# Optimization experiments

Measured on AMD Instinct MI355X. Metric: run time of the kernel, lower is better.

Reference implementation:

```python
import jax, jax.numpy as jnp
import numpy as np

B, G, K, H, NC = 128, 12000, 512, 64, 100
FP = 2048
ALPHA = 0.1
STEPS = 10

def setup_inputs() -> dict:
    key = jax.random.key(0)
    ks = jax.random.split(key, 10)
    ctl = jax.random.normal(ks[0], (B, G), jnp.float32)
    # drug targets: sparse binary indicator per gene
    drug_targets = (jax.random.uniform(ks[1], (B, G)) < 0.01).astype(jnp.float32)
    cell_idx = jax.random.randint(ks[2], (B,), 0, NC, dtype=jnp.int32)
    drug_fp = jax.random.normal(ks[3], (B, FP), jnp.float32)  # unused in forward
    # gene->module membership (sparse-ish binary), ensure each module non-empty via deg clamp in model
    M = (jax.random.uniform(ks[4], (G, K)) < 0.02).astype(jnp.float32)
    # row-stochastic module adjacency for stable diffusion
    Araw = jax.random.uniform(ks[5], (K, K), jnp.float32)
    A = Araw / jnp.sum(Araw, axis=1, keepdims=True)
    W_in = jax.random.normal(ks[6], (2, H), jnp.float32) * 0.5
    b_in = jnp.zeros((H,), jnp.float32)
    cell_emb = jax.random.normal(ks[7], (NC, H), jnp.float32) * 0.02
    W_out = jax.random.normal(ks[8], (H, 1), jnp.float32) * 0.1
    b_out = jnp.zeros((1,), jnp.float32)
    return {"ctl": ctl, "drug_targets": drug_targets, "cell_idx": cell_idx,
            "drug_fp": drug_fp, "M": M, "A": A, "W_in": W_in, "b_in": b_in,
            "cell_emb": cell_emb, "W_out": W_out, "b_out": b_out}

def reference(ctl, drug_targets, cell_idx, drug_fp, M, A, W_in, b_in, cell_emb, W_out, b_out):
    # module degree (clamped) as in __init__
    mod_deg = jnp.maximum(jnp.sum(M, axis=0), 1.0)            # [K]
    x_gene = jnp.stack([ctl, drug_targets], axis=-1)          # [B,G,2]
    x_mod = jnp.einsum('gk,bgh->bkh', M, x_gene) / mod_deg[None, :, None]  # [B,K,2]
    S = jax.nn.relu(x_mod @ W_in + b_in)                      # [B,K,H]
    # 10-step personalized-PageRank-style diffusion over modules
    def step(Z, _):
        Z = (1.0 - ALPHA) * jnp.einsum('bkh,kl->blh', Z, A) + ALPHA * S
        return Z, None
    Z, _ = jax.lax.scan(step, S, None, length=STEPS)          # [B,K,H]
    h_gene = jnp.einsum('gk,bkh->bgh', M, Z)                  # [B,G,H]
    h_gene = h_gene + cell_emb[cell_idx][:, None, :]          # add cell embedding
    y = (h_gene @ W_out + b_out)[..., 0]                      # [B,G]
    return y
```

## Files before the change

### kernel.cpp

```cpp
#include <hip/hip_runtime.h>

#define B_    128
#define G_    12000
#define GP    12288
#define K_    512
#define H_    64
#define NSEG  24
#define SEGG  512
#define BKT   64
#define NGT   192

typedef __attribute__((ext_vector_type(8))) short bf16x8;
typedef __attribute__((ext_vector_type(4))) float f32x4;

__device__ __forceinline__ unsigned short f2bf(float x) {
    union { float f; unsigned u; } v; v.f = x;
    unsigned r = (v.u + 0x7FFFu + ((v.u >> 16) & 1u)) >> 16;
    return (unsigned short)r;
}
__device__ __forceinline__ float bf2f(unsigned short b) {
    union { float f; unsigned u; } v; v.u = ((unsigned)b) << 16;
    return v.f;
}

__device__ __forceinline__ void mm_body(int k0, int l0, float* __restrict__ sm,
        const float* __restrict__ Aop, const float* __restrict__ Bop,
        const float* __restrict__ Cop, const float* __restrict__ Dop,
        float alpha, float beta, float* __restrict__ O, float* __restrict__ O2) {
    float (*Xa)[68] = (float(*)[68])sm;
    float (*Xb)[36] = (float(*)[36])(sm + 2176);
    int tid = threadIdx.x;
    int kg = tid & 15, lg = tid >> 4;
    float acc[2][2] = {};
    for (int jj = 0; jj < K_; jj += 64) {
#pragma unroll
        for (int i = 0; i < 2; ++i) {
            int lin = tid + i * 256;
            int r = lin >> 4, c4 = lin & 15;
            *(float4*)&Xa[r][c4 * 4] =
                *(const float4*)&Aop[(size_t)(l0 + r) * K_ + jj + c4 * 4];
        }
#pragma unroll
        for (int i = 0; i < 2; ++i) {
            int lin = tid + i * 256;
            int r = lin >> 3, c4 = lin & 7;
            *(float4*)&Xb[r][c4 * 4] =
                *(const float4*)&Bop[(size_t)(jj + r) * K_ + k0 + c4 * 4];
        }
        __syncthreads();
#pragma unroll 8
        for (int j = 0; j < 64; ++j) {
            float xa0 = Xa[lg * 2][j], xa1 = Xa[lg * 2 + 1][j];
            float xb0 = Xb[j][kg * 2], xb1 = Xb[j][kg * 2 + 1];
            acc[0][0] = fmaf(xa0, xb0, acc[0][0]);
            acc[0][1] = fmaf(xa0, xb1, acc[0][1]);
            acc[1][0] = fmaf(xa1, xb0, acc[1][0]);
            acc[1][1] = fmaf(xa1, xb1, acc[1][1]);
        }
        __syncthreads();
    }
#pragma unroll
    for (int i = 0; i < 2; ++i) {
        size_t idx = (size_t)(l0 + lg * 2 + i) * K_ + k0 + kg * 2;
        float2 v;
        v.x = alpha * acc[i][0];
        v.y = alpha * acc[i][1];
        if (beta != 0.0f) {
            float2 cc = *(const float2*)&Cop[idx];
            v.x = fmaf(beta, cc.x, v.x);
            v.y = fmaf(beta, cc.y, v.y);
        }
        *(float2*)&O[idx] = v;
        if (O2) {
            float2 dd = *(const float2*)&Dop[idx];
            float2 w2; w2.x = v.x + dd.x; w2.y = v.y + dd.y;
            *(float2*)&O2[idx] = w2;
        }
    }
}

__device__ __forceinline__ void panel_body(int l, float* __restrict__ sm,
        const float* __restrict__ W, const float* __restrict__ src,
        float* __restrict__ out) {
    float* Wr  = sm;
    float* red = sm + 512;
    int tid = threadIdx.x;
    if (tid < 128)
        ((float4*)Wr)[tid] = ((const float4*)&W[(size_t)l * K_])[tid];
    __syncthreads();
    int b = tid & 127, seg = tid >> 7;
    int kb = seg * 256;
    float a0 = 0.f, a1 = 0.f, a2 = 0.f, a3 = 0.f;
#pragma unroll 4
    for (int kk = 0; kk < 256; kk += 4) {
        int k = kb + kk;
        a0 = fmaf(Wr[k + 0], src[(k + 0) * B_ + b], a0);
        a1 = fmaf(Wr[k + 1], src[(k + 1) * B_ + b], a1);
        a2 = fmaf(Wr[k + 2], src[(k + 2) * B_ + b], a2);
        a3 = fmaf(Wr[k + 3], src[(k + 3) * B_ + b], a3);
    }
    red[seg * 128 + b] = (a0 + a1) + (a2 + a3);
    __syncthreads();
    if (tid < 128)
        out[l * B_ + b] = red[b] + red[128 + b];
}

__global__ __launch_bounds__(256) void k_pre(
        const float* __restrict__ ctl, const float* __restrict__ dt,
        const float* __restrict__ M, const float* __restrict__ A,
        const int* __restrict__ cidx, const float* __restrict__ cemb,
        const float* __restrict__ W_out, const float* __restrict__ b_out,
        unsigned short* __restrict__ XpT, unsigned short* __restrict__ MTb,
        unsigned short* __restrict__ Mb, int* __restrict__ pdeg,
        float* __restrict__ AT, float* __restrict__ U2,
        float* __restrict__ cvec) {
    int bid = blockIdx.x, tid = threadIdx.x;
    if (bid < 3072) {
        int p = bid / 12, chunk = bid % 12;
        int ch = p >> 7, b = p & 127;
        const float* src = (ch ? dt : ctl) + (size_t)b * G_;
        int g = chunk * 1024 + tid * 4;
        float x0 = 0.f, x1 = 0.f, x2 = 0.f, x3 = 0.f;
        if (g + 3 < G_) {
            float4 v = *(const float4*)&src[g];
            x0 = v.x; x1 = v.y; x2 = v.z; x3 = v.w;
        } else {
            if (g + 0 < G_) x0 = src[g + 0];
            if (g + 1 < G_) x1 = src[g + 1];
            if (g + 2 < G_) x2 = src[g + 2];
            if (g + 3 < G_) x3 = src[g + 3];
        }
        ushort4 hv;
        hv.x = f2bf(x0); hv.y = f2bf(x1); hv.z = f2bf(x2); hv.w = f2bf(x3);
        *(ushort4*)&XpT[(size_t)p * GP + g] = hv;
    } else if (bid < 4608) {
        __shared__ float t[64][65];
        __shared__ int csum[4][64];
        int id = bid - 3072;
        int gt = id % NGT, kt = id / NGT;
        int g0 = gt * 64, k0 = kt * 64;
        int tx = tid & 63, ty = tid >> 6;
        int cnt = 0;
#pragma unroll
        for (int j = 0; j < 16; ++j) {
            int g = g0 + ty + 4 * j;
            float v = (g < G_) ? M[(size_t)g * K_ + k0 + tx] : 0.0f;
            t[ty + 4 * j][tx] = v;
            Mb[(size_t)g * K_ + k0 + tx] = f2bf(v);
            cnt += (v != 0.0f);
        }
        csum[ty][tx] = cnt;
        __syncthreads();
        if (ty == 0)
            pdeg[(size_t)(k0 + tx) * NGT + gt] =
                csum[0][tx] + csum[1][tx] + csum[2][tx] + csum[3][tx];
#pragma unroll
        for (int j = 0; j < 16; ++j)
            MTb[(size_t)(k0 + ty + 4 * j) * GP + g0 + tx] =
                f2bf(t[tx][ty + 4 * j]);
    } else if (bid < 4864) {
        __shared__ float t[32][33];
        int id = bid - 4608;
        int x0 = (id & 15) * 32, y0 = (id >> 4) * 32;
        int tx = tid & 31, ty = tid >> 5;
#pragma unroll
        for (int j = 0; j < 4; ++j)
            t[ty + 8 * j][tx] = A[(size_t)(y0 + ty + 8 * j) * K_ + x0 + tx];
        __syncthreads();
#pragma unroll
        for (int j = 0; j < 4; ++j) {
            int row = x0 + ty + 8 * j, col = y0 + tx;
            float v = t[tx][ty + 8 * j];
            AT[(size_t)row * K_ + col] = v;
            U2[(size_t)row * K_ + col] = 0.09f * v + (row == col ? 0.1f : 0.0f);
        }
    } else {
        if (tid < B_) {
            int ci = cidx[tid];
            float acc = b_out[0];
#pragma unroll 8
            for (int h = 0; h < H_; ++h)
                acc = fmaf(cemb[ci * H_ + h], W_out[h], acc);
            cvec[tid] = acc;
        }
    }
}

__global__ __launch_bounds__(256) void k_gemm(
        const unsigned short* __restrict__ MTb, const unsigned short* __restrict__ XpT,
        float* __restrict__ Cp,
        const float* __restrict__ AT, const float* __restrict__ U2,
        float* __restrict__ M2, float* __restrict__ Yop) {
    __shared__ __align__(16) char smraw[36864];
    int bid = blockIdx.x, tid = threadIdx.x;
    if (bid < 192) {
        unsigned short (*Al)[72] = (unsigned short(*)[72])smraw;
        unsigned short (*Bl)[72] = (unsigned short(*)[72])(smraw + 18432);
        int tile = bid & 7, seg = bid >> 3;
        int m0 = (tile & 3) * 128, n0 = (tile >> 2) * 128;
        size_t gbase = (size_t)seg * SEGG;
        int wid = tid >> 6, lane = tid & 63;
        int wm = (wid >> 1) * 64, wn = (wid & 1) * 64;
        int r16 = lane & 15, kg8 = (lane >> 4) * 8;
        int ld_row = tid >> 3, ld_c8 = (tid & 7) * 8;
        f32x4 acc[4][4] = {};
        for (int kk = 0; kk < SEGG; kk += BKT) {
#pragma unroll
            for (int i = 0; i < 4; ++i) {
                int r = ld_row + 32 * i;
                *(uint4*)&Al[r][ld_c8] =
                    *(const uint4*)&MTb[(size_t)(m0 + r) * GP + gbase + kk + ld_c8];
                *(uint4*)&Bl[r][ld_c8] =
                    *(const uint4*)&XpT[(size_t)(n0 + r) * GP + gbase + kk + ld_c8];
            }
            __syncthreads();
#pragma unroll
            for (int ks = 0; ks < 2; ++ks) {
                bf16x8 af[4], bf[4];
#pragma unroll
                for (int mi = 0; mi < 4; ++mi)
                    af[mi] = *(const bf16x8*)&Al[wm + mi * 16 + r16][ks * 32 + kg8];
#pragma unroll
                for (int ni = 0; ni < 4; ++ni)
                    bf[ni] = *(const bf16x8*)&Bl[wn + ni * 16 + r16][ks * 32 + kg8];
#pragma unroll
                for (int mi = 0; mi < 4; ++mi)
#pragma unroll
                    for (int ni = 0; ni < 4; ++ni)
                        acc[mi][ni] = __builtin_amdgcn_mfma_f32_16x16x32_bf16(
                            af[mi], bf[ni], acc[mi][ni], 0, 0, 0);
            }
            __syncthreads();
        }
        float* C = Cp + (size_t)seg * (K_ * 256);
        int cr = (lane >> 4) * 4, cc = lane & 15;
#pragma unroll
        for (int mi = 0; mi < 4; ++mi)
#pragma unroll
            for (int ni = 0; ni < 4; ++ni) {
                size_t rb = (size_t)(m0 + wm + mi * 16 + cr) * 256
                          + (n0 + wn + ni * 16 + cc);
#pragma unroll
                for (int r = 0; r < 4; ++r)
                    C[rb + (size_t)r * 256] = acc[mi][ni][r];
            }
    } else {
        int id = bid - 192;
        mm_body((id & 15) * 32, (id >> 4) * 32, (float*)smraw,
                AT, AT, nullptr, U2, 0.81f, 0.0f, M2, Yop);
    }
}

__global__ __launch_bounds__(256) void k_red(
        const float* __restrict__ Cp, const int* __restrict__ pdeg,
        const float* __restrict__ W_in, const float* __restrict__ b_in,
        const float* __restrict__ W_out, float* __restrict__ sout,
        const float* __restrict__ M2, const float* __restrict__ U2,
        float* __restrict__ M4, float* __restrict__ U4) {
    __shared__ __align__(16) float sm[4480];
    int bid = blockIdx.x, tid = threadIdx.x;
    if (bid < 256) {
        int kloc = tid >> 7, b = tid & 127;
        int k = bid * 2 + kloc;
        int v = 0;
        if (b < 96)
            v = pdeg[(size_t)k * NGT + b] + pdeg[(size_t)k * NGT + 96 + b];
#pragma unroll
        for (int off = 32; off; off >>= 1) v += __shfl_down(v, off, 64);
        __shared__ int dsum[4];
        __shared__ float degs[2];
        if ((tid & 63) == 0) dsum[tid >> 6] = v;
        __syncthreads();
        if (tid < 2) degs[tid] = (float)(dsum[tid * 2] + dsum[tid * 2 + 1]);
        __syncthreads();
        float x0 = 0.f, x1 = 0.f;
#pragma unroll 4
        for (int s = 0; s < NSEG; ++s) {
            const float* Cb = Cp + (size_t)s * (K_ * 256) + (size_t)k * 256;
            x0 += Cb[b];
            x1 += Cb[128 + b];
        }
        float inv = 1.0f / fmaxf(degs[kloc], 1.0f);
        x0 *= inv; x1 *= inv;
        float s = 0.f;
#pragma unroll 8
        for (int h = 0; h < H_; ++h) {
            float vv = fmaf(x0, W_in[h], fmaf(x1, W_in[H_ + h], b_in[h]));
            vv = fmaxf(vv, 0.f);
            s = fmaf(vv, W_out[h], s);
        }
        sout[k * B_ + b] = s;
    } else {
        int id = bid - 256;
        int t = id & 255;
        if (id < 256)
            mm_body((t & 15) * 32, (t >> 4) * 32, sm, M2, M2, nullptr, nullptr,
                    1.0f, 0.0f, M4, nullptr);
        else
            mm_body((t & 15) * 32, (t >> 4) * 32, sm, M2, U2, U2, nullptr,
                    1.0f, 1.0f, U4, nullptr);
    }
}

__global__ __launch_bounds__(256) void k_p3(
        const float* __restrict__ M4, const float* __restrict__ U4,
        float* __restrict__ M8,
        const float* __restrict__ Yop, const float* __restrict__ sout,
        float* __restrict__ q, float* __restrict__ bb) {
    __shared__ __align__(16) float sm[4480];
    int bid = blockIdx.x;
    if (bid < 256) {
        mm_body((bid & 15) * 32, (bid >> 4) * 32, sm, M4, M4, nullptr, nullptr,
                1.0f, 0.0f, M8, nullptr);
    } else if (bid < 768) {
        panel_body(bid - 256, sm, Yop, sout, q);
    } else {
        panel_body(bid - 768, sm, U4, sout, bb);
    }
}

__global__ __launch_bounds__(1024) void k_zfin(
        const float* __restrict__ M8, const float* __restrict__ M4,
        const float* __restrict__ q, const float* __restrict__ bb,
        unsigned short* __restrict__ zbT) {
    __shared__ __align__(16) float Wr[4 * K_];
    __shared__ float red[8][2][128];
    int tid = threadIdx.x;
    int l0 = blockIdx.x * 2;
    if (tid < 256)
        ((float4*)Wr)[tid] = ((const float4*)&M8[(size_t)l0 * K_])[tid];
    else if (tid < 512)
        ((float4*)&Wr[2 * K_])[tid - 256] =
            ((const float4*)&M4[(size_t)l0 * K_])[tid - 256];
    __syncthreads();
    int b = tid & 127, seg = tid >> 7;
    int kb = seg * 64;
    float a0m = 0.f, a0u = 0.f, a1m = 0.f, a1u = 0.f;
#pragma unroll 8
    for (int kk = 0; kk < 64; ++kk) {
        int k = kb + kk;
        float qv = q[k * B_ + b];
        float bv = bb[k * B_ + b];
        a0m = fmaf(Wr[k], qv, a0m);
        a0u = fmaf(Wr[2 * K_ + k], bv, a0u);
        a1m = fmaf(Wr[K_ + k], qv, a1m);
        a1u = fmaf(Wr[3 * K_ + k], bv, a1u);
    }
    red[seg][0][b] = a0m + a0u;
    red[seg][1][b] = a1m + a1u;
    __syncthreads();
    if (tid < 256) {
        int row = tid >> 7, bi = tid & 127;
        float t = bb[(l0 + row) * B_ + bi];
#pragma unroll
        for (int u = 0; u < 8; ++u) t += red[u][row][bi];
        unsigned short hi = f2bf(t);
        unsigned short lo = f2bf(t - bf2f(hi));
        zbT[(size_t)bi * (2 * K_) + (l0 + row)]      = hi;
        zbT[(size_t)bi * (2 * K_) + K_ + (l0 + row)] = lo;
    }
}

__global__ __launch_bounds__(256) void k_yg(
        const unsigned short* __restrict__ Mb, const unsigned short* __restrict__ zbT,
        const float* __restrict__ cvec, float* __restrict__ y) {
    __shared__ __align__(16) unsigned short Al[64][72];
    __shared__ __align__(16) unsigned short Bh[128][72];
    __shared__ __align__(16) unsigned short Bl2[128][72];
    int tid = threadIdx.x;
    int g0 = blockIdx.x * 64;
    int wid = tid >> 6, lane = tid & 63;
    int wm = (wid >> 1) * 32, wn = (wid & 1) * 64;
    int r16 = lane & 15, kg8 = (lane >> 4) * 8;
    int ld_row = tid >> 3, ld_c8 = (tid & 7) * 8;
    f32x4 acc[2][4] = {};
    for (int kk = 0; kk < K_; kk += BKT) {
#pragma unroll
        for (int i = 0; i < 2; ++i) {
            int r = ld_row + 32 * i;
            *(uint4*)&Al[r][ld_c8] =
                *(const uint4*)&Mb[(size_t)(g0 + r) * K_ + kk + ld_c8];
        }
#pragma unroll
        for (int i = 0; i < 4; ++i) {
            int r = ld_row + 32 * i;
            *(uint4*)&Bh[r][ld_c8] =
                *(const uint4*)&zbT[(size_t)r * (2 * K_) + kk + ld_c8];
            *(uint4*)&Bl2[r][ld_c8] =
                *(const uint4*)&zbT[(size_t)r * (2 * K_) + K_ + kk + ld_c8];
        }
        __syncthreads();
#pragma unroll
        for (int ks = 0; ks < 2; ++ks) {
            bf16x8 af[2], bh[4], bl[4];
#pragma unroll
            for (int mi = 0; mi < 2; ++mi)
                af[mi] = *(const bf16x8*)&Al[wm + mi * 16 + r16][ks * 32 + kg8];
#pragma unroll
            for (int ni = 0; ni < 4; ++ni) {
                bh[ni] = *(const bf16x8*)&Bh[wn + ni * 16 + r16][ks * 32 + kg8];
                bl[ni] = *(const bf16x8*)&Bl2[wn + ni * 16 + r16][ks * 32 + kg8];
            }
#pragma unroll
            for (int mi = 0; mi < 2; ++mi)
#pragma unroll
                for (int ni = 0; ni < 4; ++ni) {
                    acc[mi][ni] = __builtin_amdgcn_mfma_f32_16x16x32_bf16(
                        af[mi], bh[ni], acc[mi][ni], 0, 0, 0);
                    acc[mi][ni] = __builtin_amdgcn_mfma_f32_16x16x32_bf16(
                        af[mi], bl[ni], acc[mi][ni], 0, 0, 0);
                }
        }
        __syncthreads();
    }
    int cr = (lane >> 4) * 4, cc = lane & 15;
#pragma unroll
    for (int ni = 0; ni < 4; ++ni) {
        int b = wn + ni * 16 + cc;
        float cv = cvec[b];
#pragma unroll
        for (int mi = 0; mi < 2; ++mi) {
            int g = g0 + wm + mi * 16 + cr;
            if (g < G_) {
                float4 o;
                o.x = acc[mi][ni][0] + cv;
                o.y = acc[mi][ni][1] + cv;
                o.z = acc[mi][ni][2] + cv;
                o.w = acc[mi][ni][3] + cv;
                *(float4*)&y[(size_t)b * G_ + g] = o;
            }
        }
    }
}

extern "C" void kernel_launch(void* const* d_in, const int* in_sizes, int n_in,
                              void* d_out, int out_size, void* d_ws, size_t ws_size,
                              hipStream_t stream) {
    const float* ctl   = (const float*)d_in[0];
    const float* dt    = (const float*)d_in[1];
    const int*   cidx  = (const int*)d_in[2];
    const float* M     = (const float*)d_in[4];
    const float* A     = (const float*)d_in[5];
    const float* W_in  = (const float*)d_in[6];
    const float* b_in  = (const float*)d_in[7];
    const float* cemb  = (const float*)d_in[8];
    const float* W_out = (const float*)d_in[9];
    const float* b_out = (const float*)d_in[10];
    float* y = (float*)d_out;

    char* ws = (char*)d_ws;
    size_t o = 0;
    auto take = [&](size_t bytes) { char* p = ws + o; o = (o + bytes + 255) & ~(size_t)255; return p; };
    unsigned short* XpT = (unsigned short*)take((size_t)256 * GP * 2);
    unsigned short* MTb = (unsigned short*)take((size_t)K_ * GP * 2);
    unsigned short* Mb  = (unsigned short*)take((size_t)GP * K_ * 2);
    unsigned short* zbT = (unsigned short*)take((size_t)B_ * 2 * K_ * 2);
    float* Cp   = (float*)take((size_t)NSEG * K_ * 256 * 4);
    int*   pdeg = (int*)  take((size_t)K_ * NGT * 4);
    float* cvec = (float*)take(B_ * 4);
    float* AT   = (float*)take((size_t)K_ * K_ * 4);
    float* U2   = (float*)take((size_t)K_ * K_ * 4);
    float* M2   = (float*)take((size_t)K_ * K_ * 4);
    float* Yop  = (float*)take((size_t)K_ * K_ * 4);
    float* M4   = (float*)take((size_t)K_ * K_ * 4);
    float* U4   = (float*)take((size_t)K_ * K_ * 4);
    float* M8   = (float*)take((size_t)K_ * K_ * 4);
    float* sout = (float*)take((size_t)K_ * B_ * 4);
    float* q    = (float*)take((size_t)K_ * B_ * 4);
    float* bb   = (float*)take((size_t)K_ * B_ * 4);
    (void)ws_size; (void)in_sizes; (void)n_in; (void)out_size;

    k_pre<<<4865, 256, 0, stream>>>(ctl, dt, M, A, cidx, cemb, W_out, b_out,
                                    XpT, MTb, Mb, pdeg, AT, U2, cvec);
    k_gemm<<<448, 256, 0, stream>>>(MTb, XpT, Cp, AT, U2, M2, Yop);
    k_red<<<768, 256, 0, stream>>>(Cp, pdeg, W_in, b_in, W_out, sout,
                                   M2, U2, M4, U4);
    k_p3<<<1280, 256, 0, stream>>>(M4, U4, M8, Yop, sout, q, bb);
    k_zfin<<<K_ / 2, 1024, 0, stream>>>(M8, M4, q, bb, zbT);
    k_yg<<<(G_ + 63) / 64, 256, 0, stream>>>(Mb, zbT, cvec, y);
}
```

Baseline: 98.73 us.

## Fuse six stage kernels into one cooperative persistent kernel with grid syncs

Replaces the six separate kernel launches with a single cooperative persistent kernel of 256 blocks that loops over each stage's jobs and separates stages with grid-wide syncs, keeping the old multi-launch path as a fallback. The aim is to remove per-launch overhead and the drain/fill gaps between kernels. The zfin stage is also reworked from 1024-thread blocks handling two rows to 256-thread blocks handling one row. The risk is that 256 persistent blocks underuse the GPU on the large stages such as the 4865-job preprocessing, and grid syncs carry their own cost.

```diff
diff --git a/kernel.cpp b/kernel.cpp
--- a/kernel.cpp
+++ b/kernel.cpp
@@ -1,4 +1,7 @@
 #include <hip/hip_runtime.h>
+#include <hip/hip_cooperative_groups.h>
+
+namespace cg = cooperative_groups;
 
 #define B_    128
 #define G_    12000
@@ -9,6 +12,7 @@
 #define SEGG  512
 #define BKT   64
 #define NGT   192
+#define NB    256
 
 typedef __attribute__((ext_vector_type(8))) short bf16x8;
 typedef __attribute__((ext_vector_type(4))) float f32x4;
@@ -22,6 +26,17 @@
     union { float f; unsigned u; } v; v.u = ((unsigned)b) << 16;
     return v.f;
 }
+
+struct Params {
+    const float *ctl, *dt, *M, *A;
+    const int* cidx;
+    const float *cemb, *W_out, *b_out, *W_in, *b_in;
+    unsigned short *XpT, *MTb, *Mb, *zbT;
+    float* Cp;
+    int* pdeg;
+    float *cvec, *AT, *U2, *M2, *Yop, *M4, *U4, *M8, *sout, *q, *bb;
+    float* y;
+};
 
 __device__ __forceinline__ void mm_body(int k0, int l0, float* __restrict__ sm,
         const float* __restrict__ Aop, const float* __restrict__ Bop,
@@ -105,20 +120,12 @@
         out[l * B_ + b] = red[b] + red[128 + b];
 }
 
-__global__ __launch_bounds__(256) void k_pre(
-        const float* __restrict__ ctl, const float* __restrict__ dt,
-        const float* __restrict__ M, const float* __restrict__ A,
-        const int* __restrict__ cidx, const float* __restrict__ cemb,
-        const float* __restrict__ W_out, const float* __restrict__ b_out,
-        unsigned short* __restrict__ XpT, unsigned short* __restrict__ MTb,
-        unsigned short* __restrict__ Mb, int* __restrict__ pdeg,
-        float* __restrict__ AT, float* __restrict__ U2,
-        float* __restrict__ cvec) {
-    int bid = blockIdx.x, tid = threadIdx.x;
-    if (bid < 3072) {
-        int p = bid / 12, chunk = bid % 12;
-        int ch = p >> 7, b = p & 127;
-        const float* src = (ch ? dt : ctl) + (size_t)b * G_;
+__device__ __forceinline__ void pre_job(int j, char* smraw, const Params& p) {
+    int tid = threadIdx.x;
+    if (j < 3072) {
+        int pp = j / 12, chunk = j % 12;
+        int ch = pp >> 7, b = pp & 127;
+        const float* src = (ch ? p.dt : p.ctl) + (size_t)b * G_;
         int g = chunk * 1024 + tid * 4;
         float x0 = 0.f, x1 = 0.f, x2 = 0.f, x3 = 0.f;
         if (g + 3 < G_) {
@@ -132,243 +139,187 @@
         }
         ushort4 hv;
         hv.x = f2bf(x0); hv.y = f2bf(x1); hv.z = f2bf(x2); hv.w = f2bf(x3);
-        *(ushort4*)&XpT[(size_t)p * GP + g] = hv;
-    } else if (bid < 4608) {
-        __shared__ float t[64][65];
-        __shared__ int csum[4][64];
-        int id = bid - 3072;
+        *(ushort4*)&p.XpT[(size_t)pp * GP + g] = hv;
+    } else if (j < 4608) {
+        float (*t)[65] = (float(*)[65])smraw;
+        int (*csum)[64] = (int(*)[64])(smraw + 16640);
+        int id = j - 3072;
         int gt = id % NGT, kt = id / NGT;
         int g0 = gt * 64, k0 = kt * 64;
         int tx = tid & 63, ty = tid >> 6;
         int cnt = 0;
 #pragma unroll
-        for (int j = 0; j < 16; ++j) {
-            int g = g0 + ty + 4 * j;
-            float v = (g < G_) ? M[(size_t)g * K_ + k0 + tx] : 0.0f;
-            t[ty + 4 * j][tx] = v;
-            Mb[(size_t)g * K_ + k0 + tx] = f2bf(v);
+        for (int jj = 0; jj < 16; ++jj) {
+            int g = g0 + ty + 4 * jj;
+            float v = (g < G_) ? p.M[(size_t)g * K_ + k0 + tx] : 0.0f;
+            t[ty + 4 * jj][tx] = v;
+            p.Mb[(size_t)g * K_ + k0 + tx] = f2bf(v);
             cnt += (v != 0.0f);
         }
         csum[ty][tx] = cnt;
         __syncthreads();
         if (ty == 0)
-            pdeg[(size_t)(k0 + tx) * NGT + gt] =
+            p.pdeg[(size_t)(k0 + tx) * NGT + gt] =
                 csum[0][tx] + csum[1][tx] + csum[2][tx] + csum[3][tx];
 #pragma unroll
-        for (int j = 0; j < 16; ++j)
-            MTb[(size_t)(k0 + ty + 4 * j) * GP + g0 + tx] =
-                f2bf(t[tx][ty + 4 * j]);
-    } else if (bid < 4864) {
-        __shared__ float t[32][33];
-        int id = bid - 4608;
+        for (int jj = 0; jj < 16; ++jj)
+            p.MTb[(size_t)(k0 + ty + 4 * jj) * GP + g0 + tx] =
+                f2bf(t[tx][ty + 4 * jj]);
+    } else if (j < 4864) {
+        float (*t)[33] = (float(*)[33])smraw;
+        int id = j - 4608;
         int x0 = (id & 15) * 32, y0 = (id >> 4) * 32;
         int tx = tid & 31, ty = tid >> 5;
 #pragma unroll
-        for (int j = 0; j < 4; ++j)
-            t[ty + 8 * j][tx] = A[(size_t)(y0 + ty + 8 * j) * K_ + x0 + tx];
-        __syncthreads();
-#pragma unroll
-        for (int j = 0; j < 4; ++j) {
-            int row = x0 + ty + 8 * j, col = y0 + tx;
-            float v = t[tx][ty + 8 * j];
-            AT[(size_t)row * K_ + col] = v;
-            U2[(size_t)row * K_ + col] = 0.09f * v + (row == col ? 0.1f : 0.0f);
+        for (int jj = 0; jj < 4; ++jj)
+            t[ty + 8 * jj][tx] = p.A[(size_t)(y0 + ty + 8 * jj) * K_ + x0 + tx];
+        __syncthreads();
+#pragma unroll
+        for (int jj = 0; jj < 4; ++jj) {
+            int row = x0 + ty + 8 * jj, col = y0 + tx;
+            float v = t[tx][ty + 8 * jj];
+            p.AT[(size_t)row * K_ + col] = v;
+            p.U2[(size_t)row * K_ + col] = 0.09f * v + (row == col ? 0.1f : 0.0f);
         }
     } else {
         if (tid < B_) {
-            int ci = cidx[tid];
-            float acc = b_out[0];
+            int ci = p.cidx[tid];
+            float acc = p.b_out[0];
 #pragma unroll 8
             for (int h = 0; h < H_; ++h)
-                acc = fmaf(cemb[ci * H_ + h], W_out[h], acc);
-            cvec[tid] = acc;
-        }
-    }
-}
-
-__global__ __launch_bounds__(256) void k_gemm(
-        const unsigned short* __restrict__ MTb, const unsigned short* __restrict__ XpT,
-        float* __restrict__ Cp,
-        const float* __restrict__ AT, const float* __restrict__ U2,
-        float* __restrict__ M2, float* __restrict__ Yop) {
-    __shared__ __align__(16) char smraw[36864];
-    int bid = blockIdx.x, tid = threadIdx.x;
-    if (bid < 192) {
-        unsigned short (*Al)[72] = (unsigned short(*)[72])smraw;
-        unsigned short (*Bl)[72] = (unsigned short(*)[72])(smraw + 18432);
-        int tile = bid & 7, seg = bid >> 3;
-        int m0 = (tile & 3) * 128, n0 = (tile >> 2) * 128;
-        size_t gbase = (size_t)seg * SEGG;
-        int wid = tid >> 6, lane = tid & 63;
-        int wm = (wid >> 1) * 64, wn = (wid & 1) * 64;
-        int r16 = lane & 15, kg8 = (lane >> 4) * 8;
-        int ld_row = tid >> 3, ld_c8 = (tid & 7) * 8;
-        f32x4 acc[4][4] = {};
-        for (int kk = 0; kk < SEGG; kk += BKT) {
-#pragma unroll
-            for (int i = 0; i < 4; ++i) {
-                int r = ld_row + 32 * i;
-                *(uint4*)&Al[r][ld_c8] =
-                    *(const uint4*)&MTb[(size_t)(m0 + r) * GP + gbase + kk + ld_c8];
-                *(uint4*)&Bl[r][ld_c8] =
-                    *(const uint4*)&XpT[(size_t)(n0 + r) * GP + gbase + kk + ld_c8];
-            }
-            __syncthreads();
-#pragma unroll
-            for (int ks = 0; ks < 2; ++ks) {
-                bf16x8 af[4], bf[4];
-#pragma unroll
-                for (int mi = 0; mi < 4; ++mi)
-                    af[mi] = *(const bf16x8*)&Al[wm + mi * 16 + r16][ks * 32 + kg8];
+                acc = fmaf(p.cemb[ci * H_ + h], p.W_out[h], acc);
+            p.cvec[tid] = acc;
+        }
+    }
+}
+
+__device__ __forceinline__ void gemm_job(int j, char* smraw, const Params& p) {
+    unsigned short (*Al)[72] = (unsigned short(*)[72])smraw;
+    unsigned short (*Bl)[72] = (unsigned short(*)[72])(smraw + 18432);
+    int tid = threadIdx.x;
+    int tile = j & 7, seg = j >> 3;
+    int m0 = (tile & 3) * 128, n0 = (tile >> 2) * 128;
+    size_t gbase = (size_t)seg * SEGG;
+    int wid = tid >> 6, lane = tid & 63;
+    int wm = (wid >> 1) * 64, wn = (wid & 1) * 64;
+    int r16 = lane & 15, kg8 = (lane >> 4) * 8;
+    int ld_row = tid >> 3, ld_c8 = (tid & 7) * 8;
+    f32x4 acc[4][4] = {};
+    for (int kk = 0; kk < SEGG; kk += BKT) {
+#pragma unroll
+        for (int i = 0; i < 4; ++i) {
+            int r = ld_row + 32 * i;
+            *(uint4*)&Al[r][ld_c8] =
+                *(const uint4*)&p.MTb[(size_t)(m0 + r) * GP + gbase + kk + ld_c8];
+            *(uint4*)&Bl[r][ld_c8] =
+                *(const uint4*)&p.XpT[(size_t)(n0 + r) * GP + gbase + kk + ld_c8];
+        }
+        __syncthreads();
+#pragma unroll
+        for (int ks = 0; ks < 2; ++ks) {
+            bf16x8 af[4], bf[4];
+#pragma unroll
+            for (int mi = 0; mi < 4; ++mi)
+                af[mi] = *(const bf16x8*)&Al[wm + mi * 16 + r16][ks * 32 + kg8];
+#pragma unroll
+            for (int ni = 0; ni < 4; ++ni)
+                bf[ni] = *(const bf16x8*)&Bl[wn + ni * 16 + r16][ks * 32 + kg8];
+#pragma unroll
+            for (int mi = 0; mi < 4; ++mi)
 #pragma unroll
                 for (int ni = 0; ni < 4; ++ni)
-                    bf[ni] = *(const bf16x8*)&Bl[wn + ni * 16 + r16][ks * 32 + kg8];
-#pragma unroll
-                for (int mi = 0; mi < 4; ++mi)
-#pragma unroll
-                    for (int ni = 0; ni < 4; ++ni)
-                        acc[mi][ni] = __builtin_amdgcn_mfma_f32_16x16x32_bf16(
-                            af[mi], bf[ni], acc[mi][ni], 0, 0, 0);
-            }
-            __syncthreads();
-        }
-        float* C = Cp + (size_t)seg * (K_ * 256);
-        int cr = (lane >> 4) * 4, cc = lane & 15;
-#pragma unroll
-        for (int mi = 0; mi < 4; ++mi)
-#pragma unroll
-            for (int ni = 0; ni < 4; ++ni) {
-                size_t rb = (size_t)(m0 + wm + mi * 16 + cr) * 256
-                          + (n0 + wn + ni * 16 + cc);
-#pragma unroll
-                for (int r = 0; r < 4; ++r)
-                    C[rb + (size_t)r * 256] = acc[mi][ni][r];
-            }
-    } else {
-        int id = bid - 192;
-        mm_body((id & 15) * 32, (id >> 4) * 32, (float*)smraw,
-                AT, AT, nullptr, U2, 0.81f, 0.0f, M2, Yop);
-    }
-}
-
-__global__ __launch_bounds__(256) void k_red(
-        const float* __restrict__ Cp, const int* __restrict__ pdeg,
-        const float* __restrict__ W_in, const float* __restrict__ b_in,
-        const float* __restrict__ W_out, float* __restrict__ sout,
-        const float* __restrict__ M2, const float* __restrict__ U2,
-        float* __restrict__ M4, float* __restrict__ U4) {
-    __shared__ __align__(16) float sm[4480];
-    int bid = blockIdx.x, tid = threadIdx.x;
-    if (bid < 256) {
-        int kloc = tid >> 7, b = tid & 127;
-        int k = bid * 2 + kloc;
-        int v = 0;
-        if (b < 96)
-            v = pdeg[(size_t)k * NGT + b] + pdeg[(size_t)k * NGT + 96 + b];
-#pragma unroll
-        for (int off = 32; off; off >>= 1) v += __shfl_down(v, off, 64);
-        __shared__ int dsum[4];
-        __shared__ float degs[2];
-        if ((tid & 63) == 0) dsum[tid >> 6] = v;
-        __syncthreads();
-        if (tid < 2) degs[tid] = (float)(dsum[tid * 2] + dsum[tid * 2 + 1]);
-        __syncthreads();
-        float x0 = 0.f, x1 = 0.f;
+                    acc[mi][ni] = __builtin_amdgcn_mfma_f32_16x16x32_bf16(
+                        af[mi], bf[ni], acc[mi][ni], 0, 0, 0);
+        }
+        __syncthreads();
+    }
+    float* C = p.Cp + (size_t)seg * (K_ * 256);
+    int cr = (lane >> 4) * 4, cc = lane & 15;
+#pragma unroll
+    for (int mi = 0; mi < 4; ++mi)
+#pragma unroll
+        for (int ni = 0; ni < 4; ++ni) {
+            size_t rb = (size_t)(m0 + wm + mi * 16 + cr) * 256
+                      + (n0 + wn + ni * 16 + cc);
+#pragma unroll
+            for (int r = 0; r < 4; ++r)
+                C[rb + (size_t)r * 256] = acc[mi][ni][r];
+        }
+}
+
+__device__ __forceinline__ void red_job(int j, const Params& p) {
+    __shared__ int dsum[4];
+    __shared__ float degs[2];
+    int tid = threadIdx.x;
+    int kloc = tid >> 7, b = tid & 127;
+    int k = j * 2 + kloc;
+    int v = 0;
+    if (b < 96)
+        v = p.pdeg[(size_t)k * NGT + b] + p.pdeg[(size_t)k * NGT + 96 + b];
+#pragma unroll
+    for (int off = 32; off; off >>= 1) v += __shfl_down(v, off, 64);
+    if ((tid & 63) == 0) dsum[tid >> 6] = v;
+    __syncthreads();
+    if (tid < 2) degs[tid] = (float)(dsum[tid * 2] + dsum[tid * 2 + 1]);
+    __syncthreads();
+    float x0 = 0.f, x1 = 0.f;
 #pragma unroll 4
-        for (int s = 0; s < NSEG; ++s) {
-            const float* Cb = Cp + (size_t)s * (K_ * 256) + (size_t)k * 256;
-            x0 += Cb[b];
-            x1 += Cb[128 + b];
-        }
-        float inv = 1.0f / fmaxf(degs[kloc], 1.0f);
-        x0 *= inv; x1 *= inv;
-        float s = 0.f;
+    for (int s = 0; s < NSEG; ++s) {
+        const float* Cb = p.Cp + (size_t)s * (K_ * 256) + (size_t)k * 256;
+        x0 += Cb[b];
+        x1 += Cb[128 + b];
+    }
+    float inv = 1.0f / fmaxf(degs[kloc], 1.0f);
+    x0 *= inv; x1 *= inv;
+    float s = 0.f;
 #pragma unroll 8
-        for (int h = 0; h < H_; ++h) {
-            float vv = fmaf(x0, W_in[h], fmaf(x1, W_in[H_ + h], b_in[h]));
-            vv = fmaxf(vv, 0.f);
-            s = fmaf(vv, W_out[h], s);
-        }
-        sout[k * B_ + b] = s;
-    } else {
-        int id = bid - 256;
-        int t = id & 255;
-        if (id < 256)
-            mm_body((t & 15) * 32, (t >> 4) * 32, sm, M2, M2, nullptr, nullptr,
-                    1.0f, 0.0f, M4, nullptr);
-        else
-            mm_body((t & 15) * 32, (t >> 4) * 32, sm, M2, U2, U2, nullptr,
-                    1.0f, 1.0f, U4, nullptr);
-    }
-}
-
-__global__ __launch_bounds__(256) void k_p3(
-        const float* __restrict__ M4, const float* __restrict__ U4,
-        float* __restrict__ M8,
-        const float* __restrict__ Yop, const float* __restrict__ sout,
-        float* __restrict__ q, float* __restrict__ bb) {
-    __shared__ __align__(16) float sm[4480];
-    int bid = blockIdx.x;
-    if (bid < 256) {
-        mm_body((bid & 15) * 32, (bid >> 4) * 32, sm, M4, M4, nullptr, nullptr,
-                1.0f, 0.0f, M8, nullptr);
-    } else if (bid < 768) {
-        panel_body(bid - 256, sm, Yop, sout, q);
-    } else {
-        panel_body(bid - 768, sm, U4, sout, bb);
-    }
-}
-
-__global__ __launch_bounds__(1024) void k_zfin(
-        const float* __restrict__ M8, const float* __restrict__ M4,
-        const float* __restrict__ q, const float* __restrict__ bb,
-        unsigned short* __restrict__ zbT) {
-    __shared__ __align__(16) float Wr[4 * K_];
-    __shared__ float red[8][2][128];
-    int tid = threadIdx.x;
-    int l0 = blockIdx.x * 2;
-    if (tid < 256)
-        ((float4*)Wr)[tid] = ((const float4*)&M8[(size_t)l0 * K_])[tid];
-    else if (tid < 512)
-        ((float4*)&Wr[2 * K_])[tid - 256] =
-            ((const float4*)&M4[(size_t)l0 * K_])[tid - 256];
+    for (int h = 0; h < H_; ++h) {
+        float vv = fmaf(x0, p.W_in[h], fmaf(x1, p.W_in[H_ + h], p.b_in[h]));
+        vv = fmaxf(vv, 0.f);
+        s = fmaf(vv, p.W_out[h], s);
+    }
+    p.sout[k * B_ + b] = s;
+    __syncthreads();
+}
+
+__device__ __forceinline__ void zfin_job(int l, char* smraw, const Params& p) {
+    float* Wr  = (float*)smraw;
+    float* red = (float*)smraw + 1024;
+    int tid = threadIdx.x;
+    if (tid < 128)
+        ((float4*)Wr)[tid] = ((const float4*)&p.M8[(size_t)l * K_])[tid];
+    else
+        ((float4*)Wr)[tid] = ((const float4*)&p.M4[(size_t)l * K_])[tid - 128];
     __syncthreads();
     int b = tid & 127, seg = tid >> 7;
-    int kb = seg * 64;
-    float a0m = 0.f, a0u = 0.f, a1m = 0.f, a1u = 0.f;
-#pragma unroll 8
-    for (int kk = 0; kk < 64; ++kk) {
+    int kb = seg * 256;
+    float a0 = 0.f, a1 = 0.f, a2 = 0.f, a3 = 0.f;
+#pragma unroll 4
+    for (int kk = 0; kk < 256; kk += 2) {
         int k = kb + kk;
-        float qv = q[k * B_ + b];
-        float bv = bb[k * B_ + b];
-        a0m = fmaf(Wr[k], qv, a0m);
-        a0u = fmaf(Wr[2 * K_ + k], bv, a0u);
-        a1m = fmaf(Wr[K_ + k], qv, a1m);
-        a1u = fmaf(Wr[3 * K_ + k], bv, a1u);
-    }
-    red[seg][0][b] = a0m + a0u;
-    red[seg][1][b] = a1m + a1u;
-    __syncthreads();
-    if (tid < 256) {
-        int row = tid >> 7, bi = tid & 127;
-        float t = bb[(l0 + row) * B_ + bi];
-#pragma unroll
-        for (int u = 0; u < 8; ++u) t += red[u][row][bi];
+        a0 = fmaf(Wr[k],           p.q [(size_t)k * B_ + b], a0);
+        a1 = fmaf(Wr[512 + k],     p.bb[(size_t)k * B_ + b], a1);
+        a2 = fmaf(Wr[k + 1],       p.q [(size_t)(k + 1) * B_ + b], a2);
+        a3 = fmaf(Wr[512 + k + 1], p.bb[(size_t)(k + 1) * B_ + b], a3);
+    }
+    red[seg * 128 + b] = (a0 + a1) + (a2 + a3);
+    __syncthreads();
+    if (tid < 128) {
+        float t = red[tid] + red[128 + tid] + p.bb[(size_t)l * B_ + tid];
         unsigned short hi = f2bf(t);
         unsigned short lo = f2bf(t - bf2f(hi));
-        zbT[(size_t)bi * (2 * K_) + (l0 + row)]      = hi;
-        zbT[(size_t)bi * (2 * K_) + K_ + (l0 + row)] = lo;
-    }
-}
-
-__global__ __launch_bounds__(256) void k_yg(
-        const unsigned short* __restrict__ Mb, const unsigned short* __restrict__ zbT,
-        const float* __restrict__ cvec, float* __restrict__ y) {
-    __shared__ __align__(16) unsigned short Al[64][72];
-    __shared__ __align__(16) unsigned short Bh[128][72];
-    __shared__ __align__(16) unsigned short Bl2[128][72];
-    int tid = threadIdx.x;
-    int g0 = blockIdx.x * 64;
+        p.zbT[(size_t)tid * (2 * K_) + l]      = hi;
+        p.zbT[(size_t)tid * (2 * K_) + K_ + l] = lo;
+    }
+    __syncthreads();
+}
+
+__device__ __forceinline__ void yg_job(int j, char* smraw, const Params& p) {
+    unsigned short (*Al)[72]  = (unsigned short(*)[72])smraw;
+    unsigned short (*Bh)[72]  = (unsigned short(*)[72])(smraw + 9216);
+    unsigned short (*Bl2)[72] = (unsigned short(*)[72])(smraw + 27648);
+    int tid = threadIdx.x;
+    int g0 = j * 64;
     int wid = tid >> 6, lane = tid & 63;
     int wm = (wid >> 1) * 32, wn = (wid & 1) * 64;
     int r16 = lane & 15, kg8 = (lane >> 4) * 8;
@@ -379,15 +330,15 @@
         for (int i = 0; i < 2; ++i) {
             int r = ld_row + 32 * i;
             *(uint4*)&Al[r][ld_c8] =
-                *(const uint4*)&Mb[(size_t)(g0 + r) * K_ + kk + ld_c8];
+                *(const uint4*)&p.Mb[(size_t)(g0 + r) * K_ + kk + ld_c8];
         }
 #pragma unroll
         for (int i = 0; i < 4; ++i) {
             int r = ld_row + 32 * i;
             *(uint4*)&Bh[r][ld_c8] =
-                *(const uint4*)&zbT[(size_t)r * (2 * K_) + kk + ld_c8];
+                *(const uint4*)&p.zbT[(size_t)r * (2 * K_) + kk + ld_c8];
             *(uint4*)&Bl2[r][ld_c8] =
-                *(const uint4*)&zbT[(size_t)r * (2 * K_) + K_ + kk + ld_c8];
+                *(const uint4*)&p.zbT[(size_t)r * (2 * K_) + K_ + kk + ld_c8];
         }
         __syncthreads();
 #pragma unroll
@@ -417,7 +368,7 @@
 #pragma unroll
     for (int ni = 0; ni < 4; ++ni) {
         int b = wn + ni * 16 + cc;
-        float cv = cvec[b];
+        float cv = p.cvec[b];
 #pragma unroll
         for (int mi = 0; mi < 2; ++mi) {
             int g = g0 + wm + mi * 16 + cr;
@@ -427,55 +378,160 @@
                 o.y = acc[mi][ni][1] + cv;
                 o.z = acc[mi][ni][2] + cv;
                 o.w = acc[mi][ni][3] + cv;
-                *(float4*)&y[(size_t)b * G_ + g] = o;
+                *(float4*)&p.y[(size_t)b * G_ + g] = o;
             }
         }
     }
+}
+
+__global__ __launch_bounds__(256, 2) void k_mega(Params p) {
+    static __shared__ __align__(16) char smem[46080];
+    cg::grid_group grid = cg::this_grid();
+    float* smf = (float*)smem;
+
+    for (int j = blockIdx.x; j < 4865; j += NB) {
+        __syncthreads();
+        pre_job(j, smem, p);
+    }
+    grid.sync();
+    for (int j = blockIdx.x; j < 448; j += NB) {
+        __syncthreads();
+        if (j < 192) gemm_job(j, smem, p);
+        else {
+            int id = j - 192;
+            mm_body((id & 15) * 32, (id >> 4) * 32, smf,
+                    p.AT, p.AT, nullptr, p.U2, 0.81f, 0.0f, p.M2, p.Yop);
+        }
+    }
+    grid.sync();
+    for (int j = blockIdx.x; j < 768; j += NB) {
+        __syncthreads();
+        if (j < 256) red_job(j, p);
+        else if (j < 512) {
+            int t = j - 256;
+            mm_body((t & 15) * 32, (t >> 4) * 32, smf, p.M2, p.M2,
+                    nullptr, nullptr, 1.0f, 0.0f, p.M4, nullptr);
+        } else {
+            int t = j - 512;
+            mm_body((t & 15) * 32, (t >> 4) * 32, smf, p.M2, p.U2,
+                    p.U2, nullptr, 1.0f, 1.0f, p.U4, nullptr);
+        }
+    }
+    grid.sync();
+    for (int j = blockIdx.x; j < 1280; j += NB) {
+        __syncthreads();
+        if (j < 256)
+            mm_body((j & 15) * 32, (j >> 4) * 32, smf, p.M4, p.M4,
+                    nullptr, nullptr, 1.0f, 0.0f, p.M8, nullptr);
+        else if (j < 768) panel_body(j - 256, smf, p.Yop, p.sout, p.q);
+        else              panel_body(j - 768, smf, p.U4, p.sout, p.bb);
+    }
+    grid.sync();
+    for (int j = blockIdx.x; j < 512; j += NB) {
+        __syncthreads();
+        zfin_job(j, smem, p);
+    }
+    grid.sync();
+    for (int j = blockIdx.x; j < (G_ + 63) / 64; j += NB) {
+        __syncthreads();
+        yg_job(j, smem, p);
+    }
+}
+
+__global__ __launch_bounds__(256) void kf_pre(Params p) {
+    static __shared__ __align__(16) char smem[17664];
+    pre_job(blockIdx.x, smem, p);
+}
+__global__ __launch_bounds__(256) void kf_gemm(Params p) {
+    static __shared__ __align__(16) char smem[36864];
+    int j = blockIdx.x;
+    if (j < 192) gemm_job(j, smem, p);
+    else {
+        int id = j - 192;
+        mm_body((id & 15) * 32, (id >> 4) * 32, (float*)smem,
+                p.AT, p.AT, nullptr, p.U2, 0.81f, 0.0f, p.M2, p.Yop);
+    }
+}
+__global__ __launch_bounds__(256) void kf_red(Params p) {
+    static __shared__ __align__(16) char smem[17920];
+    int j = blockIdx.x;
+    if (j < 256) red_job(j, p);
+    else if (j < 512) {
+        int t = j - 256;
+        mm_body((t & 15) * 32, (t >> 4) * 32, (float*)smem, p.M2, p.M2,
+                nullptr, nullptr, 1.0f, 0.0f, p.M4, nullptr);
+    } else {
+        int t = j - 512;
+        mm_body((t & 15) * 32, (t >> 4) * 32, (float*)smem, p.M2, p.U2,
+                p.U2, nullptr, 1.0f, 1.0f, p.U4, nullptr);
+    }
+}
+__global__ __launch_bounds__(256) void kf_p3(Params p) {
+    static __shared__ __align__(16) char smem[17920];
+    int j = blockIdx.x;
+    if (j < 256)
+        mm_body((j & 15) * 32, (j >> 4) * 32, (float*)smem, p.M4, p.M4,
+                nullptr, nullptr, 1.0f, 0.0f, p.M8, nullptr);
+    else if (j < 768) panel_body(j - 256, (float*)smem, p.Yop, p.sout, p.q);
+    else              panel_body(j - 768, (float*)smem, p.U4, p.sout, p.bb);
+}
+__global__ __launch_bounds__(256) void kf_zfin(Params p) {
+    static __shared__ __align__(16) char smem[5120];
+    zfin_job(blockIdx.x, smem, p);
+}
+__global__ __launch_bounds__(256) void kf_yg(Params p) {
+    static __shared__ __align__(16) char smem[46080];
+    yg_job(blockIdx.x, smem, p);
 }
 
 extern "C" void kernel_launch(void* const* d_in, const int* in_sizes, int n_in,
                               void* d_out, int out_size, void* d_ws, size_t ws_size,
                               hipStream_t stream) {
-    const float* ctl   = (const float*)d_in[0];
-    const float* dt    = (const float*)d_in[1];
-    const int*   cidx  = (const int*)d_in[2];
-    const float* M     = (const float*)d_in[4];
-    const float* A     = (const float*)d_in[5];
-    const float* W_in  = (const float*)d_in[6];
-    const float* b_in  = (const float*)d_in[7];
-    const float* cemb  = (const float*)d_in[8];
-    const float* W_out = (const float*)d_in[9];
-    const float* b_out = (const float*)d_in[10];
-    float* y = (float*)d_out;
+    Params p;
+    p.ctl   = (const float*)d_in[0];
+    p.dt    = (const float*)d_in[1];
+    p.cidx  = (const int*)d_in[2];
+    p.M     = (const float*)d_in[4];
+    p.A     = (const float*)d_in[5];
+    p.W_in  = (const float*)d_in[6];
+    p.b_in  = (const float*)d_in[7];
+    p.cemb  = (const float*)d_in[8];
+    p.W_out = (const float*)d_in[9];
+    p.b_out = (const float*)d_in[10];
+    p.y     = (float*)d_out;
 
     char* ws = (char*)d_ws;
     size_t o = 0;
-    auto take = [&](size_t bytes) { char* p = ws + o; o = (o + bytes + 255) & ~(size_t)255; return p; };
-    unsigned short* XpT = (unsigned short*)take((size_t)256 * GP * 2);
-    unsigned short* MTb = (unsigned short*)take((size_t)K_ * GP * 2);
-    unsigned short* Mb  = (unsigned short*)take((size_t)GP * K_ * 2);
-    unsigned short* zbT = (unsigned short*)take((size_t)B_ * 2 * K_ * 2);
-    float* Cp   = (float*)take((size_t)NSEG * K_ * 256 * 4);
-    int*   pdeg = (int*)  take((size_t)K_ * NGT * 4);
-    float* cvec = (float*)take(B_ * 4);
-    float* AT   = (float*)take((size_t)K_ * K_ * 4);
-    float* U2   = (float*)take((size_t)K_ * K_ * 4);
-    float* M2   = (float*)take((size_t)K_ * K_ * 4);
-    float* Yop  = (float*)take((size_t)K_ * K_ * 4);
-    float* M4   = (float*)take((size_t)K_ * K_ * 4);
-    float* U4   = (float*)take((size_t)K_ * K_ * 4);
-    float* M8   = (float*)take((size_t)K_ * K_ * 4);
-    float* sout = (float*)take((size_t)K_ * B_ * 4);
-    float* q    = (float*)take((size_t)K_ * B_ * 4);
-    float* bb   = (float*)take((size_t)K_ * B_ * 4);
+    auto take = [&](size_t bytes) { char* q = ws + o; o = (o + bytes + 255) & ~(size_t)255; return q; };
+    p.XpT  = (unsigned short*)take((size_t)256 * GP * 2);
+    p.MTb  = (unsigned short*)take((size_t)K_ * GP * 2);
+    p.Mb   = (unsigned short*)take((size_t)GP * K_ * 2);
+    p.zbT  = (unsigned short*)take((size_t)B_ * 2 * K_ * 2);
+    p.Cp   = (float*)take((size_t)NSEG * K_ * 256 * 4);
+    p.pdeg = (int*)  take((size_t)K_ * NGT * 4);
+    p.cvec = (float*)take(B_ * 4);
+    p.AT   = (float*)take((size_t)K_ * K_ * 4);
+    p.U2   = (float*)take((size_t)K_ * K_ * 4);
+    p.M2   = (float*)take((size_t)K_ * K_ * 4);
+    p.Yop  = (float*)take((size_t)K_ * K_ * 4);
+    p.M4   = (float*)take((size_t)K_ * K_ * 4);
+    p.U4   = (float*)take((size_t)K_ * K_ * 4);
+    p.M8   = (float*)take((size_t)K_ * K_ * 4);
+    p.sout = (float*)take((size_t)K_ * B_ * 4);
+    p.q    = (float*)take((size_t)K_ * B_ * 4);
+    p.bb   = (float*)take((size_t)K_ * B_ * 4);
     (void)ws_size; (void)in_sizes; (void)n_in; (void)out_size;
 
-    k_pre<<<4865, 256, 0, stream>>>(ctl, dt, M, A, cidx, cemb, W_out, b_out,
-                                    XpT, MTb, Mb, pdeg, AT, U2, cvec);
-    k_gemm<<<448, 256, 0, stream>>>(MTb, XpT, Cp, AT, U2, M2, Yop);
-    k_red<<<768, 256, 0, stream>>>(Cp, pdeg, W_in, b_in, W_out, sout,
-                                   M2, U2, M4, U4);
-    k_p3<<<1280, 256, 0, stream>>>(M4, U4, M8, Yop, sout, q, bb);
-    k_zfin<<<K_ / 2, 1024, 0, stream>>>(M8, M4, q, bb, zbT);
-    k_yg<<<(G_ + 63) / 64, 256, 0, stream>>>(Mb, zbT, cvec, y);
-}
+    void* args[] = { &p };
+    hipError_t err = hipLaunchCooperativeKernel((void*)k_mega, dim3(NB),
+                                                dim3(256), args, 0, stream);
+    if (err != hipSuccess) {
+        (void)hipGetLastError();
+        kf_pre <<<4865, 256, 0, stream>>>(p);
+        kf_gemm<<<448,  256, 0, stream>>>(p);
+        kf_red <<<768,  256, 0, stream>>>(p);
+        kf_p3  <<<1280, 256, 0, stream>>>(p);
+        kf_zfin<<<512,  256, 0, stream>>>(p);
+        kf_yg  <<<(G_ + 63) / 64, 256, 0, stream>>>(p);
+    }
+}
```

Measured after the change: 338.7 us. 3.43x slower.
